# Performance work log

Hardware: AMD Instinct MI355X
Metric: run time of the kernel (lower is better)

## Reference

```python
import jax, jax.numpy as jnp
import numpy as np


def _sage_conv(x, edge_index, Wp, bp, Wl, bl, Wr):
    """PyG SAGEConv with project=True, aggr='mean', root_weight=True.
    Message side: relu(x @ Wp + bp); root side uses UNprojected x.
    """
    N = x.shape[0]
    xp = jax.nn.relu(x @ Wp + bp)                      # [N, F_in]
    src, dst = edge_index[0], edge_index[1]
    agg = jax.ops.segment_sum(xp[src], dst, num_segments=N)   # [N, F_in]
    cnt = jax.ops.segment_sum(jnp.ones(src.shape, x.dtype), dst, num_segments=N)
    mean = agg / jnp.maximum(cnt, 1.0)[:, None]        # mean aggr; 0 for isolated nodes
    return mean @ Wl + bl + x @ Wr                     # lin_l(aggr) + lin_r(root)


def setup_inputs() -> dict:
    key = jax.random.key(0)
    ks = jax.random.split(key, 16)
    BS, NUM_NODES = 16, 5000
    N = BS * NUM_NODES            # 80000 total nodes
    F_IN, HID, REP = 256, 256, 128
    E = 1_280_000                 # avg degree 16
    K = 2500                      # kriging targets per batch element

    def w(k, shape):
        return jax.random.normal(k, shape, jnp.float32) * 0.02

    return {
        "x": jax.random.normal(ks[0], (N, F_IN), jnp.float32),
        "edge_index": jax.random.randint(ks[1], (2, E), 0, N),
        "map_id": jax.random.randint(ks[2], (BS, K), 0, NUM_NODES),
        "bs": BS,
        # SAGEConv 1: in=256 -> out=256
        "Wp1": w(ks[3], (F_IN, F_IN)), "bp1": jnp.zeros((F_IN,), jnp.float32),
        "Wl1": w(ks[4], (F_IN, HID)),  "bl1": jnp.zeros((HID,), jnp.float32),
        "Wr1": w(ks[5], (F_IN, HID)),
        # SAGEConv 2: in=256 -> out=128
        "Wp2": w(ks[6], (HID, HID)),   "bp2": jnp.zeros((HID,), jnp.float32),
        "Wl2": w(ks[7], (HID, REP)),   "bl2": jnp.zeros((REP,), jnp.float32),
        "Wr2": w(ks[8], (HID, REP)),
        # final Linear rep -> rep
        "Wlin": w(ks[9], (REP, REP)),  "blin": jnp.zeros((REP,), jnp.float32),
    }


def reference(x, edge_index, map_id, bs,
              Wp1, bp1, Wl1, bl1, Wr1,
              Wp2, bp2, Wl2, bl2, Wr2,
              Wlin, blin):
    h = jax.nn.relu(_sage_conv(x, edge_index, Wp1, bp1, Wl1, bl1, Wr1))
    h = jax.nn.relu(_sage_conv(h, edge_index, Wp2, bp2, Wl2, bl2, Wr2))
    h = h @ Wlin + blin                                # [N, rep]
    num_nodes = x.shape[0] // bs
    rep = h.shape[1]
    h3 = h.reshape(bs, num_nodes, rep)
    # gather kriging-target node features per batch element
    local_feat = jnp.take_along_axis(h3, map_id[:, :, None], axis=1).reshape(-1, rep)
    return (local_feat, h)
```

## Files before the change

### kernel.cpp

```cpp
#include <hip/hip_runtime.h>
#include <hip/hip_bf16.h>

typedef __attribute__((ext_vector_type(8))) short s16x8;
typedef __attribute__((ext_vector_type(8))) ushort u16x8;
typedef __attribute__((ext_vector_type(4))) float f32x4;

static __device__ __forceinline__ float b2f(ushort u) {
  union { float f; unsigned bits; } v; v.bits = ((unsigned)u) << 16; return v.f;
}
static __device__ __forceinline__ ushort f2b(float f) {
  __hip_bfloat16 h = __float2bfloat16(f);
  return *reinterpret_cast<ushort*>(&h);
}

__global__ void detect_dtype(const ushort* __restrict__ xraw, int* __restrict__ flag) {
  __shared__ int cnt;
  if (threadIdx.x == 0) cnt = 0;
  __syncthreads();
  ushort u = xraw[threadIdx.x];
  int e = (u >> 7) & 0xFF;
  if (e >= 113 && e <= 141) atomicAdd(&cnt, 1);
  __syncthreads();
  if (threadIdx.x == 0) *flag = (cnt >= 224) ? 0 : 1;
}

__global__ void convert_x(const void* __restrict__ xin, ushort* __restrict__ xb,
                          const int* __restrict__ flag, int n) {
  int i = blockIdx.x * 256 + threadIdx.x;
  int base = i * 8;
  if (base >= n) return;
  if (*flag) {
    const float4 v0 = ((const float4*)xin)[i * 2];
    const float4 v1 = ((const float4*)xin)[i * 2 + 1];
    u16x8 o;
    o[0] = f2b(v0.x); o[1] = f2b(v0.y); o[2] = f2b(v0.z); o[3] = f2b(v0.w);
    o[4] = f2b(v1.x); o[5] = f2b(v1.y); o[6] = f2b(v1.z); o[7] = f2b(v1.w);
    ((u16x8*)xb)[i] = o;
  } else {
    ((u16x8*)xb)[i] = ((const u16x8*)xin)[i];
  }
}

struct WDesc { const void* src; ushort* dst; int R, C; };
struct WPack { WDesc d[7]; };

__global__ void transpose_convert_all(WPack p, const int* __restrict__ flag) {
  const WDesc& d = p.d[blockIdx.y];
  int i = blockIdx.x * 256 + threadIdx.x;
  if (i >= d.R * d.C) return;
  int r = i / d.C, c = i % d.C;
  ushort v = (*flag) ? f2b(((const float*)d.src)[i]) : ((const ushort*)d.src)[i];
  d.dst[c * d.R + r] = v;
}

struct BPack { WDesc d[5]; };
__global__ void convert_vec_all(BPack p, const int* __restrict__ flag) {
  const WDesc& d = p.d[blockIdx.y];
  int i = threadIdx.x;
  if (i >= d.R) return;
  d.dst[i] = (*flag) ? f2b(((const float*)d.src)[i]) : ((const ushort*)d.src)[i];
}

__global__ __launch_bounds__(256)
void hist_bucket_kernel(const int* __restrict__ dst, int* __restrict__ deg,
                        int* __restrict__ bcnt, int E, int N, int nbuck) {
  __shared__ int lh[512];
  int t = threadIdx.x;
  for (int i = t; i < nbuck; i += 256) lh[i] = 0;
  __syncthreads();
  int base = blockIdx.x * 2048;
#pragma unroll
  for (int k = 0; k < 8; ++k) {
    int e = base + k * 256 + t;
    if (e < E) {
      unsigned d = (unsigned)dst[e];
      if (d < (unsigned)N) {
        atomicAdd(&deg[d], 1);
        atomicAdd(&lh[d >> 9], 1);
      }
    }
  }
  __syncthreads();
  for (int i = t; i < nbuck; i += 256)
    if (lh[i]) atomicAdd(&bcnt[i], lh[i]);
}

__global__ __launch_bounds__(256)
void scan_buckets(const int* __restrict__ bcnt, int* __restrict__ bscan,
                  int* __restrict__ bpos, int nbuck) {
  int t = threadIdx.x;
  __shared__ int sh[256];
  int v = (t < nbuck) ? bcnt[t] : 0;
  sh[t] = v; __syncthreads();
  for (int off = 1; off < 256; off <<= 1) {
    int u = (t >= off) ? sh[t - off] : 0;
    __syncthreads();
    sh[t] += u;
    __syncthreads();
  }
  if (t < nbuck) { int ex = sh[t] - v; bscan[t] = ex; bpos[t] = ex; }
  if (t == nbuck - 1) bscan[nbuck] = sh[t];
}

__global__ __launch_bounds__(256)
void bin_scatter(const int* __restrict__ src, const int* __restrict__ dstl,
                 int* __restrict__ bpos, int2* __restrict__ pairs,
                 int E, int N, int nbuck) {
  __shared__ int lh[512];
  __shared__ int lbase[512];
  int t = threadIdx.x;
  for (int i = t; i < nbuck; i += 256) lh[i] = 0;
  __syncthreads();
  int base = blockIdx.x * 4096;
#pragma unroll
  for (int k = 0; k < 16; ++k) {
    int e = base + k * 256 + t;
    if (e < E) {
      unsigned d = (unsigned)dstl[e];
      if (d < (unsigned)N) atomicAdd(&lh[d >> 9], 1);
    }
  }
  __syncthreads();
  for (int i = t; i < nbuck; i += 256) {
    int c = lh[i];
    lbase[i] = c ? atomicAdd(&bpos[i], c) : 0;
    lh[i] = 0;
  }
  __syncthreads();
#pragma unroll
  for (int k = 0; k < 16; ++k) {
    int e = base + k * 256 + t;
    if (e < E) {
      unsigned d = (unsigned)dstl[e];
      if (d < (unsigned)N) {
        int b = d >> 9;
        int r = atomicAdd(&lh[b], 1);
        pairs[lbase[b] + r] = make_int2(src[e], (int)d);
      }
    }
  }
}

#define FS_SPLIT 4
__global__ __launch_bounds__(256)
void final_scatter(const int2* __restrict__ pairs, const int* __restrict__ bscan,
                   int* __restrict__ pos, int* __restrict__ eidx, int E) {
  int b = blockIdx.x / FS_SPLIT;
  int part = blockIdx.x % FS_SPLIT;
  int s = bscan[b], e = bscan[b + 1];
  int len = e - s;
  int per = (len + FS_SPLIT - 1) / FS_SPLIT;
  int lo = s + part * per;
  int hi = min(lo + per, e);
  for (int i = lo + threadIdx.x; i < hi; i += 256) {
    int2 p = pairs[i];
    unsigned q = (unsigned)atomicAdd(&pos[p.y], 1);
    if (q < (unsigned)E) eidx[q] = p.x;
  }
}

__global__ __launch_bounds__(256)
void scan_phaseA(const int* __restrict__ deg, int* __restrict__ bsum, int N) {
  int b = blockIdx.x, t = threadIdx.x;
  int i0 = b * 1024 + t * 4;
  int s = 0;
#pragma unroll
  for (int k = 0; k < 4; ++k) {
    int i = i0 + k;
    if (i < N) s += deg[i];
  }
  __shared__ int red[256];
  red[t] = s; __syncthreads();
  for (int off = 128; off > 0; off >>= 1) {
    if (t < off) red[t] += red[t + off];
    __syncthreads();
  }
  if (t == 0) bsum[b] = red[0];
}

__global__ __launch_bounds__(256)
void scan_phaseB(const int* __restrict__ bsum, int* __restrict__ ebsum,
                 int* __restrict__ rowptr, int B, int N) {
  int t = threadIdx.x;
  __shared__ int sh[256];
  int v = (t < B) ? bsum[t] : 0;
  sh[t] = v; __syncthreads();
  for (int off = 1; off < 256; off <<= 1) {
    int u = (t >= off) ? sh[t - off] : 0;
    __syncthreads();
    sh[t] += u;
    __syncthreads();
  }
  if (t < B) ebsum[t] = sh[t] - v;
  if (t == B - 1) rowptr[N] = sh[t];
}

__global__ __launch_bounds__(256)
void scan_phaseC(const int* __restrict__ deg, const int* __restrict__ ebsum,
                 int* __restrict__ rowptr, int* __restrict__ pos, int N) {
  int b = blockIdx.x, t = threadIdx.x;
  int i0 = b * 1024 + t * 4;
  int v[4]; int s = 0;
#pragma unroll
  for (int k = 0; k < 4; ++k) {
    int i = i0 + k;
    v[k] = (i < N) ? deg[i] : 0;
    s += v[k];
  }
  __shared__ int sh[256];
  sh[t] = s; __syncthreads();
  for (int off = 1; off < 256; off <<= 1) {
    int u = (t >= off) ? sh[t - off] : 0;
    __syncthreads();
    sh[t] += u;
    __syncthreads();
  }
  int run = ebsum[b] + sh[t] - s;
#pragma unroll
  for (int k = 0; k < 4; ++k) {
    int i = i0 + k;
    if (i < N) { rowptr[i] = run; pos[i] = run; run += v[k]; }
  }
}

__global__ __launch_bounds__(256)
void agg_mean_v3(const ushort* __restrict__ xp, const int* __restrict__ rowptr,
                 const int* __restrict__ eidx, ushort* __restrict__ mean, int NN) {
  int node = blockIdx.x * 4 + (threadIdx.x >> 6);
  if (node >= NN) return;
  int lane = threadIdx.x & 63;
  int half = lane >> 5;
  int l32 = lane & 31;
  int s = rowptr[node], e = rowptr[node + 1];
  float a[8];
#pragma unroll
  for (int k = 0; k < 8; ++k) a[k] = 0.f;

  for (int base = s; base < e; base += 64) {
    int cnt = min(64, e - base);
    int my = (lane < cnt) ? eidx[base + lane] : 0;
    int full = cnt >> 1;
#pragma unroll 2
    for (int it = 0; it < full; ++it) {
      int sn = __shfl(my, 2 * it + half);
      u16x8 v = *(const u16x8*)&xp[(size_t)sn * 256 + l32 * 8];
#pragma unroll
      for (int k = 0; k < 8; ++k) a[k] += b2f(v[k]);
    }
    if (cnt & 1) {
      int sn = __shfl(my, cnt - 1);
      if (half == 0) {
        u16x8 v = *(const u16x8*)&xp[(size_t)sn * 256 + l32 * 8];
#pragma unroll
        for (int k = 0; k < 8; ++k) a[k] += b2f(v[k]);
      }
    }
  }
#pragma unroll
  for (int k = 0; k < 8; ++k) a[k] += __shfl_xor(a[k], 32);

  int c = e - s; if (c < 1) c = 1;
  float inv = 1.f / (float)c;
  if (half == 0) {
    u16x8 o;
#pragma unroll
    for (int k = 0; k < 8; ++k) o[k] = f2b(a[k] * inv);
    *(u16x8*)&mean[(size_t)node * 256 + l32 * 8] = o;
  }
}

#define GLD16(g, l) \
  __builtin_amdgcn_global_load_lds((const __attribute__((address_space(1))) void*)(g), \
                                   (__attribute__((address_space(3))) void*)(l), 16, 0, 0)

__global__ __launch_bounds__(256, 3)
void gemm_bf16(const ushort* __restrict__ A1, const ushort* __restrict__ B1,
               const ushort* __restrict__ A2, const ushort* __restrict__ B2,
               const ushort* __restrict__ bias, ushort* __restrict__ C,
               int M, int N, int K1, int K2, int do_relu) {
  __shared__ __align__(16) ushort lsAB[2][128 * 64];
  const int tid = threadIdx.x;
  const int lane = tid & 63;
  const int wid = tid >> 6;
  const int wr = wid >> 1, wc = wid & 1;
  const int m0 = blockIdx.x * 128;
  const int n0 = blockIdx.y * 128;
  const int l15 = lane & 15;
  const int lg = lane >> 4;
  const int so = tid * 16;
  const int fragswz = (l15 & 7) << 4;

  f32x4 acc[4][4];
#pragma unroll
  for (int i = 0; i < 4; ++i)
#pragma unroll
    for (int j = 0; j < 4; ++j) {
      acc[i][j][0] = 0.f; acc[i][j][1] = 0.f; acc[i][j][2] = 0.f; acc[i][j][3] = 0.f;
    }

#pragma unroll
  for (int pass = 0; pass < 2; ++pass) {
    const ushort* A = pass ? A2 : A1;
    const ushort* B = pass ? B2 : B1;
    const int K = pass ? K2 : K1;
    if (K == 0) continue;
    for (int k0 = 0; k0 < K; k0 += 64) {
#pragma unroll
      for (int it = 0; it < 4; ++it) {
        int o = so + it * 4096;
        int row = o >> 7;
        int colb = o & 127;
        int gcolb = colb ^ ((row & 7) << 4);
        const ushort* ga = A + (size_t)(m0 + row) * K + k0 + (gcolb >> 1);
        GLD16(ga, (char*)lsAB[0] + o);
        const ushort* gb = B + (size_t)(n0 + row) * K + k0 + (gcolb >> 1);
        GLD16(gb, (char*)lsAB[1] + o);
      }
      __syncthreads();
#pragma unroll
      for (int kk = 0; kk < 2; ++kk) {
        const int cb = ((kk * 64 + lg * 16) ^ fragswz) >> 1;
        s16x8 af[4], bfr[4];
#pragma unroll
        for (int i = 0; i < 4; ++i)
          af[i] = *(const s16x8*)&lsAB[0][(wr * 64 + i * 16 + l15) * 64 + cb];
#pragma unroll
        for (int j = 0; j < 4; ++j)
          bfr[j] = *(const s16x8*)&lsAB[1][(wc * 64 + j * 16 + l15) * 64 + cb];
#pragma unroll
        for (int i = 0; i < 4; ++i)
#pragma unroll
          for (int j = 0; j < 4; ++j)
            acc[i][j] = __builtin_amdgcn_mfma_f32_16x16x32_bf16(af[i], bfr[j], acc[i][j], 0, 0, 0);
      }
      __syncthreads();
    }
  }

  ushort* tile = (ushort*)lsAB;
#pragma unroll
  for (int j = 0; j < 4; ++j) {
    int col = wc * 64 + j * 16 + l15;
    float bv = bias ? b2f(bias[n0 + col]) : 0.f;
#pragma unroll
    for (int i = 0; i < 4; ++i) {
#pragma unroll
      for (int r = 0; r < 4; ++r) {
        int row = wr * 64 + i * 16 + lg * 4 + r;
        float v = acc[i][j][r] + bv;
        if (do_relu) v = fmaxf(v, 0.f);
        tile[row * 128 + (col ^ ((row & 7) << 3))] = f2b(v);
      }
    }
  }
  __syncthreads();
#pragma unroll
  for (int t = 0; t < 8; ++t) {
    int id = t * 256 + tid;
    int row = id >> 4;
    int c8 = id & 15;
    u16x8 v = *(const u16x8*)&tile[row * 128 + (c8 ^ (row & 7)) * 8];
    *(u16x8*)&C[(size_t)(m0 + row) * N + n0 + c8 * 8] = v;
  }
}

__global__ __launch_bounds__(256, 2)
void gemm_h2_final(const ushort* __restrict__ A1, const ushort* __restrict__ B1,
                   const ushort* __restrict__ A2, const ushort* __restrict__ B2,
                   const ushort* __restrict__ bias2, const ushort* __restrict__ Wlin,
                   const ushort* __restrict__ biasf,
                   ushort* __restrict__ CB, float* __restrict__ CF,
                   const int* __restrict__ flag, int K1, int K2) {
  __shared__ __align__(16) ushort lsAB[2][128 * 64];
  __shared__ __align__(16) ushort lsW[128 * 128];
  const int tid = threadIdx.x;
  const int lane = tid & 63;
  const int wid = tid >> 6;
  const int wr = wid >> 1, wc = wid & 1;
  const int m0 = blockIdx.x * 128;
  const int l15 = lane & 15;
  const int lg = lane >> 4;
  const int so = tid * 16;
  const int fragswz = (l15 & 7) << 4;
  const int fl = *flag;

#pragma unroll
  for (int it = 0; it < 8; ++it) {
    int o = so + it * 4096;
    int row = o >> 8;
    int colb = o & 255;
    int gcolb = colb ^ ((row & 7) << 4);
    GLD16(Wlin + (size_t)row * 128 + (gcolb >> 1), (char*)lsW + o);
  }

  f32x4 acc[4][4];
#pragma unroll
  for (int i = 0; i < 4; ++i)
#pragma unroll
    for (int j = 0; j < 4; ++j) {
      acc[i][j][0] = 0.f; acc[i][j][1] = 0.f; acc[i][j][2] = 0.f; acc[i][j][3] = 0.f;
    }

#pragma unroll
  for (int pass = 0; pass < 2; ++pass) {
    const ushort* A = pass ? A2 : A1;
    const ushort* B = pass ? B2 : B1;
    const int K = pass ? K2 : K1;
    for (int k0 = 0; k0 < K; k0 += 64) {
#pragma unroll
      for (int it = 0; it < 4; ++it) {
        int o = so + it * 4096;
        int row = o >> 7;
        int colb = o & 127;
        int gcolb = colb ^ ((row & 7) << 4);
        GLD16(A + (size_t)(m0 + row) * K + k0 + (gcolb >> 1), (char*)lsAB[0] + o);
        GLD16(B + (size_t)row * K + k0 + (gcolb >> 1), (char*)lsAB[1] + o);
      }
      __syncthreads();
#pragma unroll
      for (int kk = 0; kk < 2; ++kk) {
        const int cb = ((kk * 64 + lg * 16) ^ fragswz) >> 1;
        s16x8 af[4], bfr[4];
#pragma unroll
        for (int i = 0; i < 4; ++i)
          af[i] = *(const s16x8*)&lsAB[0][(wr * 64 + i * 16 + l15) * 64 + cb];
#pragma unroll
        for (int j = 0; j < 4; ++j)
          bfr[j] = *(const s16x8*)&lsAB[1][(wc * 64 + j * 16 + l15) * 64 + cb];
#pragma unroll
        for (int i = 0; i < 4; ++i)
#pragma unroll
          for (int j = 0; j < 4; ++j)
            acc[i][j] = __builtin_amdgcn_mfma_f32_16x16x32_bf16(af[i], bfr[j], acc[i][j], 0, 0, 0);
      }
      __syncthreads();
    }
  }

  ushort* tile = (ushort*)lsAB;
#pragma unroll
  for (int j = 0; j < 4; ++j) {
    int col = wc * 64 + j * 16 + l15;
    float bv = b2f(bias2[col]);
#pragma unroll
    for (int i = 0; i < 4; ++i) {
#pragma unroll
      for (int r = 0; r < 4; ++r) {
        int row = wr * 64 + i * 16 + lg * 4 + r;
        float v = fmaxf(acc[i][j][r] + bv, 0.f);
        tile[row * 128 + (col ^ ((row & 7) << 3))] = f2b(v);
      }
    }
  }
  __syncthreads();

  f32x4 acc2[4][4];
#pragma unroll
  for (int i = 0; i < 4; ++i)
#pragma unroll
    for (int j = 0; j < 4; ++j) {
      acc2[i][j][0] = 0.f; acc2[i][j][1] = 0.f; acc2[i][j][2] = 0.f; acc2[i][j][3] = 0.f;
    }
#pragma unroll
  for (int kk = 0; kk < 4; ++kk) {
    s16x8 af[4], bfr[4];
#pragma unroll
    for (int i = 0; i < 4; ++i) {
      int row = wr * 64 + i * 16 + l15;
      int cb = (kk * 32 + lg * 8) ^ ((row & 7) << 3);
      af[i] = *(const s16x8*)&tile[row * 128 + cb];
    }
#pragma unroll
    for (int j = 0; j < 4; ++j) {
      int row = wc * 64 + j * 16 + l15;
      int cb = (kk * 32 + lg * 8) ^ ((row & 7) << 3);
      bfr[j] = *(const s16x8*)&lsW[row * 128 + cb];
    }
#pragma unroll
    for (int i = 0; i < 4; ++i)
#pragma unroll
      for (int j = 0; j < 4; ++j)
        acc2[i][j] = __builtin_amdgcn_mfma_f32_16x16x32_bf16(af[i], bfr[j], acc2[i][j], 0, 0, 0);
  }
  __syncthreads();

#pragma unroll
  for (int j = 0; j < 4; ++j) {
    int col = wc * 64 + j * 16 + l15;
    float bv = b2f(biasf[col]);
#pragma unroll
    for (int i = 0; i < 4; ++i) {
#pragma unroll
      for (int r = 0; r < 4; ++r) {
        int row = wr * 64 + i * 16 + lg * 4 + r;
        tile[row * 128 + (col ^ ((row & 7) << 3))] = f2b(acc2[i][j][r] + bv);
      }
    }
  }
  __syncthreads();
#pragma unroll
  for (int t = 0; t < 8; ++t) {
    int id = t * 256 + tid;
    int row = id >> 4;
    int c8 = id & 15;
    u16x8 v = *(const u16x8*)&tile[row * 128 + (c8 ^ (row & 7)) * 8];
    size_t off = (size_t)(m0 + row) * 128 + c8 * 8;
    if (fl) {
      float4 f0, f1;
      f0.x = b2f(v[0]); f0.y = b2f(v[1]); f0.z = b2f(v[2]); f0.w = b2f(v[3]);
      f1.x = b2f(v[4]); f1.y = b2f(v[5]); f1.z = b2f(v[6]); f1.w = b2f(v[7]);
      *(float4*)&CF[off] = f0;
      *(float4*)&CF[off + 4] = f1;
    } else {
      *(u16x8*)&CB[off] = v;
    }
  }
}

__global__ void gather_out(const ushort* __restrict__ hb, const float* __restrict__ hf,
                           const int* __restrict__ map_id, void* __restrict__ dout,
                           const int* __restrict__ flag,
                           int K, int num_nodes, int total, int N) {
  int i = blockIdx.x * 256 + threadIdx.x;
  if (i >= total) return;
  int f = i & 127;
  int row = i >> 7;
  int b = row / K;
  unsigned node = (unsigned)(b * num_nodes + map_id[row]);
  bool ok = node < (unsigned)N;
  if (*flag) {
    ((float*)dout)[i] = ok ? hf[(size_t)node * 128 + f] : 0.f;
  } else {
    ((ushort*)dout)[i] = ok ? hb[(size_t)node * 128 + f] : (ushort)0;
  }
}

extern "C" void kernel_launch(void* const* d_in, const int* in_sizes, int n_in,
                              void* d_out, int out_size, void* d_ws, size_t ws_size,
                              hipStream_t stream) {
  const void* x    = d_in[0];
  const int*  ei   = (const int*)d_in[1];
  const int*  mapi = (const int*)d_in[2];
  const void* Wp1  = d_in[4];
  const void* bp1  = d_in[5];
  const void* Wl1  = d_in[6];
  const void* bl1  = d_in[7];
  const void* Wr1  = d_in[8];
  const void* Wp2  = d_in[9];
  const void* bp2  = d_in[10];
  const void* Wl2  = d_in[11];
  const void* bl2  = d_in[12];
  const void* Wr2  = d_in[13];
  const void* Wlin = d_in[14];
  const void* blin = d_in[15];

  const int NN = in_sizes[0] / 256;
  const int E  = in_sizes[1] / 2;
  const int MAPROWS = in_sizes[2];
  const int BS = 16;
  const int NUM_NODES = NN / BS;
  const int KMAP = MAPROWS / BS;
  const int NBUCK = (NN + 511) >> 9;
  const int* src = ei;
  const int* dst = ei + E;

  ushort* houtB = (ushort*)d_out + (size_t)MAPROWS * 128;
  float*  houtF = (float*)d_out + (size_t)MAPROWS * 128;
  int2* pairs = (int2*)((char*)d_out + (size_t)MAPROWS * 128 * 4);

  char* sc = (char*)d_out;
  auto carve_sc = [&](size_t bytes) {
    char* p = sc; sc += (bytes + 255) & ~(size_t)255; return p;
  };
  ushort* Wp1T  = (ushort*)carve_sc(256 * 256 * 2);
  ushort* Wl1T  = (ushort*)carve_sc(256 * 256 * 2);
  ushort* Wr1T  = (ushort*)carve_sc(256 * 256 * 2);
  ushort* Wp2T  = (ushort*)carve_sc(256 * 256 * 2);
  ushort* Wl2T  = (ushort*)carve_sc(128 * 256 * 2);
  ushort* Wr2T  = (ushort*)carve_sc(128 * 256 * 2);
  ushort* WlinT = (ushort*)carve_sc(128 * 128 * 2);
  ushort* bp1c  = (ushort*)carve_sc(256 * 2);
  ushort* bl1c  = (ushort*)carve_sc(256 * 2);
  ushort* bp2c  = (ushort*)carve_sc(256 * 2);
  ushort* bl2c  = (ushort*)carve_sc(128 * 2);
  ushort* blinc = (ushort*)carve_sc(128 * 2);
  int* deg    = (int*)carve_sc((size_t)NN * 4);
  int* rowptr = (int*)carve_sc(((size_t)NN + 1) * 4);
  int* pos    = (int*)carve_sc((size_t)NN * 4);
  int* eidx   = (int*)carve_sc((size_t)E * 4);
  int* bsum   = (int*)carve_sc(1024);
  int* ebsum  = (int*)carve_sc(1024);
  int* bcnt   = (int*)carve_sc(2048);
  int* bscan  = (int*)carve_sc(2048 + 4);
  int* bpos   = (int*)carve_sc(2048);

  char* w = (char*)d_ws;
  auto carve = [&](size_t bytes) {
    char* p = w; w += (bytes + 255) & ~(size_t)255; return p;
  };
  int*    flag = (int*)carve(256);
  ushort* xb   = (ushort*)carve((size_t)NN * 256 * 2);
  ushort* bA   = (ushort*)carve((size_t)NN * 256 * 2);
  ushort* bB   = (ushort*)carve((size_t)NN * 256 * 2);

  detect_dtype<<<dim3(1), 256, 0, stream>>>((const ushort*)x, flag);
  convert_x<<<dim3((NN * 256 / 8 + 255) / 256), 256, 0, stream>>>(x, xb, flag, NN * 256);

  WPack wp;
  wp.d[0] = {Wp1, Wp1T, 256, 256};
  wp.d[1] = {Wl1, Wl1T, 256, 256};
  wp.d[2] = {Wr1, Wr1T, 256, 256};
  wp.d[3] = {Wp2, Wp2T, 256, 256};
  wp.d[4] = {Wl2, Wl2T, 256, 128};
  wp.d[5] = {Wr2, Wr2T, 256, 128};
  wp.d[6] = {Wlin, WlinT, 128, 128};
  transpose_convert_all<<<dim3(256, 7), 256, 0, stream>>>(wp, flag);

  BPack bp;
  bp.d[0] = {bp1, bp1c, 256, 1};
  bp.d[1] = {bl1, bl1c, 256, 1};
  bp.d[2] = {bp2, bp2c, 256, 1};
  bp.d[3] = {bl2, bl2c, 128, 1};
  bp.d[4] = {blin, blinc, 128, 1};
  convert_vec_all<<<dim3(1, 5), 256, 0, stream>>>(bp, flag);

  hipMemsetAsync(deg, 0, (size_t)NN * 4, stream);
  hipMemsetAsync(bcnt, 0, 2048, stream);
  hist_bucket_kernel<<<dim3((E + 2047) / 2048), 256, 0, stream>>>(dst, deg, bcnt, E, NN, NBUCK);
  scan_buckets<<<dim3(1), 256, 0, stream>>>(bcnt, bscan, bpos, NBUCK);
  int SB = (NN + 1023) / 1024;
  scan_phaseA<<<dim3(SB), 256, 0, stream>>>(deg, bsum, NN);
  scan_phaseB<<<dim3(1), 256, 0, stream>>>(bsum, ebsum, rowptr, SB, NN);
  scan_phaseC<<<dim3(SB), 256, 0, stream>>>(deg, ebsum, rowptr, pos, NN);
  bin_scatter<<<dim3((E + 4095) / 4096), 256, 0, stream>>>(src, dst, bpos, pairs, E, NN, NBUCK);
  final_scatter<<<dim3(NBUCK * FS_SPLIT), 256, 0, stream>>>(pairs, bscan, pos, eidx, E);

  dim3 blk(256);
  dim3 g256(NN / 128, 2);
  dim3 gagg((NN + 3) / 4);

  gemm_bf16<<<g256, blk, 0, stream>>>(xb, Wp1T, nullptr, nullptr, bp1c, bA,
                                      NN, 256, 256, 0, 1);
  agg_mean_v3<<<gagg, blk, 0, stream>>>(bA, rowptr, eidx, bB, NN);
  gemm_bf16<<<g256, blk, 0, stream>>>(bB, Wl1T, xb, Wr1T, bl1c, bA,
                                      NN, 256, 256, 256, 1);

  gemm_bf16<<<g256, blk, 0, stream>>>(bA, Wp2T, nullptr, nullptr, bp2c, bB,
                                      NN, 256, 256, 0, 1);
  agg_mean_v3<<<gagg, blk, 0, stream>>>(bB, rowptr, eidx, xb, NN);

  gemm_h2_final<<<dim3(NN / 128), blk, 0, stream>>>(xb, Wl2T, bA, Wr2T, bl2c,
                                                    WlinT, blinc, houtB, houtF,
                                                    flag, 256, 256);

  int total = MAPROWS * 128;
  gather_out<<<dim3((total + 255) / 256), 256, 0, stream>>>(houtB, houtF, mapi, d_out,
                                                            flag, KMAP, NUM_NODES, total, NN);
}
```

Baseline: 473.1 us.

## Build CSR per bucket in shared memory instead of global degree scans

Drops the global per-node degree histogram and its three-kernel prefix scan. Each 512-node bucket block now computes local node counts, scans them in shared memory, writes rowptr, and scatters edge sources using shared-memory atomics instead of global atomics. This removes a memset, three launches and a large number of global atomics. In exchange there is one block per bucket, which gives less parallelism than the old four-way split, and a second pass over the pairs.

```diff
diff --git a/kernel.cpp b/kernel.cpp
--- a/kernel.cpp
+++ b/kernel.cpp
@@ -61,9 +61,10 @@
   d.dst[i] = (*flag) ? f2b(((const float*)d.src)[i]) : ((const ushort*)d.src)[i];
 }
 
+
 __global__ __launch_bounds__(256)
-void hist_bucket_kernel(const int* __restrict__ dst, int* __restrict__ deg,
-                        int* __restrict__ bcnt, int E, int N, int nbuck) {
+void hist_bucket_kernel(const int* __restrict__ dst, int* __restrict__ bcnt,
+                        int E, int N, int nbuck) {
   __shared__ int lh[512];
   int t = threadIdx.x;
   for (int i = t; i < nbuck; i += 256) lh[i] = 0;
@@ -74,10 +75,7 @@
     int e = base + k * 256 + t;
     if (e < E) {
       unsigned d = (unsigned)dst[e];
-      if (d < (unsigned)N) {
-        atomicAdd(&deg[d], 1);
-        atomicAdd(&lh[d >> 9], 1);
-      }
+      if (d < (unsigned)N) atomicAdd(&lh[d >> 9], 1);
     }
   }
   __syncthreads();
@@ -87,7 +85,8 @@
 
 __global__ __launch_bounds__(256)
 void scan_buckets(const int* __restrict__ bcnt, int* __restrict__ bscan,
-                  int* __restrict__ bpos, int nbuck) {
+                  int* __restrict__ bpos, int* __restrict__ rowptr,
+                  int nbuck, int NN) {
   int t = threadIdx.x;
   __shared__ int sh[256];
   int v = (t < nbuck) ? bcnt[t] : 0;
@@ -99,7 +98,7 @@
     __syncthreads();
   }
   if (t < nbuck) { int ex = sh[t] - v; bscan[t] = ex; bpos[t] = ex; }
-  if (t == nbuck - 1) bscan[nbuck] = sh[t];
+  if (t == nbuck - 1) { bscan[nbuck] = sh[t]; rowptr[NN] = sh[t]; }
 }
 
 __global__ __launch_bounds__(256)
@@ -141,85 +140,42 @@
   }
 }
 
-#define FS_SPLIT 4
 __global__ __launch_bounds__(256)
-void final_scatter(const int2* __restrict__ pairs, const int* __restrict__ bscan,
-                   int* __restrict__ pos, int* __restrict__ eidx, int E) {
-  int b = blockIdx.x / FS_SPLIT;
-  int part = blockIdx.x % FS_SPLIT;
+void bucket_finalize(const int2* __restrict__ pairs, const int* __restrict__ bscan,
+                     int* __restrict__ rowptr, int* __restrict__ eidx, int NN) {
+  __shared__ int hist[512];
+  __shared__ int offp[512];
+  __shared__ int sh[256];
+  int b = blockIdx.x;
+  int t = threadIdx.x;
   int s = bscan[b], e = bscan[b + 1];
-  int len = e - s;
-  int per = (len + FS_SPLIT - 1) / FS_SPLIT;
-  int lo = s + part * per;
-  int hi = min(lo + per, e);
-  for (int i = lo + threadIdx.x; i < hi; i += 256) {
-    int2 p = pairs[i];
-    unsigned q = (unsigned)atomicAdd(&pos[p.y], 1);
-    if (q < (unsigned)E) eidx[q] = p.x;
-  }
-}
-
-__global__ __launch_bounds__(256)
-void scan_phaseA(const int* __restrict__ deg, int* __restrict__ bsum, int N) {
-  int b = blockIdx.x, t = threadIdx.x;
-  int i0 = b * 1024 + t * 4;
-  int s = 0;
-#pragma unroll
-  for (int k = 0; k < 4; ++k) {
-    int i = i0 + k;
-    if (i < N) s += deg[i];
-  }
-  __shared__ int red[256];
-  red[t] = s; __syncthreads();
-  for (int off = 128; off > 0; off >>= 1) {
-    if (t < off) red[t] += red[t + off];
-    __syncthreads();
-  }
-  if (t == 0) bsum[b] = red[0];
-}
-
-__global__ __launch_bounds__(256)
-void scan_phaseB(const int* __restrict__ bsum, int* __restrict__ ebsum,
-                 int* __restrict__ rowptr, int B, int N) {
-  int t = threadIdx.x;
-  __shared__ int sh[256];
-  int v = (t < B) ? bsum[t] : 0;
-  sh[t] = v; __syncthreads();
+  hist[t] = 0; hist[t + 256] = 0;
+  __syncthreads();
+  for (int i = s + t; i < e; i += 256)
+    atomicAdd(&hist[pairs[i].y & 511], 1);
+  __syncthreads();
+  int v0 = hist[2 * t], v1 = hist[2 * t + 1];
+  int sum2 = v0 + v1;
+  sh[t] = sum2; __syncthreads();
   for (int off = 1; off < 256; off <<= 1) {
     int u = (t >= off) ? sh[t - off] : 0;
     __syncthreads();
     sh[t] += u;
     __syncthreads();
   }
-  if (t < B) ebsum[t] = sh[t] - v;
-  if (t == B - 1) rowptr[N] = sh[t];
-}
-
-__global__ __launch_bounds__(256)
-void scan_phaseC(const int* __restrict__ deg, const int* __restrict__ ebsum,
-                 int* __restrict__ rowptr, int* __restrict__ pos, int N) {
-  int b = blockIdx.x, t = threadIdx.x;
-  int i0 = b * 1024 + t * 4;
-  int v[4]; int s = 0;
-#pragma unroll
-  for (int k = 0; k < 4; ++k) {
-    int i = i0 + k;
-    v[k] = (i < N) ? deg[i] : 0;
-    s += v[k];
-  }
-  __shared__ int sh[256];
-  sh[t] = s; __syncthreads();
-  for (int off = 1; off < 256; off <<= 1) {
-    int u = (t >= off) ? sh[t - off] : 0;
-    __syncthreads();
-    sh[t] += u;
-    __syncthreads();
-  }
-  int run = ebsum[b] + sh[t] - s;
-#pragma unroll
-  for (int k = 0; k < 4; ++k) {
-    int i = i0 + k;
-    if (i < N) { rowptr[i] = run; pos[i] = run; run += v[k]; }
+  int ex = sh[t] - sum2;
+  int o0 = s + ex;
+  int o1 = o0 + v0;
+  offp[2 * t] = o0;
+  offp[2 * t + 1] = o1;
+  int node0 = b * 512 + 2 * t;
+  if (node0 <= NN)     rowptr[node0] = o0;
+  if (node0 + 1 <= NN) rowptr[node0 + 1] = o1;
+  __syncthreads();
+  for (int i = s + t; i < e; i += 256) {
+    int2 p = pairs[i];
+    int r = atomicAdd(&offp[p.y & 511], 1);
+    eidx[r] = p.x;
   }
 }
 
@@ -584,12 +540,8 @@
   ushort* bp2c  = (ushort*)carve_sc(256 * 2);
   ushort* bl2c  = (ushort*)carve_sc(128 * 2);
   ushort* blinc = (ushort*)carve_sc(128 * 2);
-  int* deg    = (int*)carve_sc((size_t)NN * 4);
   int* rowptr = (int*)carve_sc(((size_t)NN + 1) * 4);
-  int* pos    = (int*)carve_sc((size_t)NN * 4);
   int* eidx   = (int*)carve_sc((size_t)E * 4);
-  int* bsum   = (int*)carve_sc(1024);
-  int* ebsum  = (int*)carve_sc(1024);
   int* bcnt   = (int*)carve_sc(2048);
   int* bscan  = (int*)carve_sc(2048 + 4);
   int* bpos   = (int*)carve_sc(2048);
@@ -624,16 +576,11 @@
   bp.d[4] = {blin, blinc, 128, 1};
   convert_vec_all<<<dim3(1, 5), 256, 0, stream>>>(bp, flag);
 
-  hipMemsetAsync(deg, 0, (size_t)NN * 4, stream);
   hipMemsetAsync(bcnt, 0, 2048, stream);
-  hist_bucket_kernel<<<dim3((E + 2047) / 2048), 256, 0, stream>>>(dst, deg, bcnt, E, NN, NBUCK);
-  scan_buckets<<<dim3(1), 256, 0, stream>>>(bcnt, bscan, bpos, NBUCK);
-  int SB = (NN + 1023) / 1024;
-  scan_phaseA<<<dim3(SB), 256, 0, stream>>>(deg, bsum, NN);
-  scan_phaseB<<<dim3(1), 256, 0, stream>>>(bsum, ebsum, rowptr, SB, NN);
-  scan_phaseC<<<dim3(SB), 256, 0, stream>>>(deg, ebsum, rowptr, pos, NN);
+  hist_bucket_kernel<<<dim3((E + 2047) / 2048), 256, 0, stream>>>(dst, bcnt, E, NN, NBUCK);
+  scan_buckets<<<dim3(1), 256, 0, stream>>>(bcnt, bscan, bpos, rowptr, NBUCK, NN);
   bin_scatter<<<dim3((E + 4095) / 4096), 256, 0, stream>>>(src, dst, bpos, pairs, E, NN, NBUCK);
-  final_scatter<<<dim3(NBUCK * FS_SPLIT), 256, 0, stream>>>(pairs, bscan, pos, eidx, E);
+  bucket_finalize<<<dim3(NBUCK), 256, 0, stream>>>(pairs, bscan, rowptr, eidx, NN);
 
   dim3 blk(256);
   dim3 g256(NN / 128, 2);
```

Measured after the change: 400.5 us. 1.18x faster.
